# Kernel tuning notes

Measured on AMD Instinct MI355X. Metric: run time of the kernel, lower is better.

Reference implementation:

```python
import jax, jax.numpy as jnp
import numpy as np

N, E, IN, HID, H, OUT = 10000, 160000, 256, 64, 8, 16
NEG_SLOPE = 0.2  # PyG GATConv leaky_relu slope


def _layer_norm(x, g, b, eps=1e-5):
    m = x.mean(-1, keepdims=True)
    v = ((x - m) ** 2).mean(-1, keepdims=True)
    return (x - m) * jax.lax.rsqrt(v + eps) * g + b


def _gat_conv(x, src, dst, W, a_src, a_dst, bias, concat):
    # PyG GATConv: h = x @ W -> [N,H,C]; e_ij = leakyrelu(a_src.h_j + a_dst.h_i);
    # alpha = segment-softmax over incoming edges at dst; out_i = sum_j alpha_ij h_j
    n = x.shape[0]
    heads, c = a_src.shape
    h = (x @ W).reshape(n, heads, c)
    al_s = (h * a_src[None]).sum(-1)  # [N,H]
    al_d = (h * a_dst[None]).sum(-1)  # [N,H]
    e = al_s[src] + al_d[dst]         # [Etot,H]
    e = jnp.where(e > 0, e, NEG_SLOPE * e)
    m = jax.ops.segment_max(e, dst, num_segments=n)
    p = jnp.exp(e - m[dst])
    s = jax.ops.segment_sum(p, dst, num_segments=n)
    a = p / (s[dst] + 1e-16)          # [Etot,H]
    out = jax.ops.segment_sum(h[src] * a[:, :, None], dst, num_segments=n)
    out = out.reshape(n, heads * c) if concat else out.mean(axis=1)
    return out + bias


def setup_inputs() -> dict:
    key = jax.random.key(0)
    ks = jax.random.split(key, 12)
    d = {}
    d['x'] = jax.random.normal(ks[0], (N, IN), jnp.float32)
    d['edge_index'] = jax.random.randint(ks[1], (2, E), 0, N, jnp.int64)
    d['Wp'] = jax.random.normal(ks[2], (IN, HID * H), jnp.float32) * 0.05
    d['bp'] = jnp.zeros((HID * H,), jnp.float32)
    d['g0'] = jnp.ones((HID * H,), jnp.float32)
    d['b0'] = jnp.zeros((HID * H,), jnp.float32)
    d['W1'] = jax.random.normal(ks[3], (HID * H, HID * H), jnp.float32) * 0.05
    d['as1'] = jax.random.normal(ks[4], (H, HID), jnp.float32) * 0.1
    d['ad1'] = jax.random.normal(ks[5], (H, HID), jnp.float32) * 0.1
    d['b1'] = jnp.zeros((HID * H,), jnp.float32)
    d['g1'] = jnp.ones((HID * H,), jnp.float32)
    d['be1'] = jnp.zeros((HID * H,), jnp.float32)
    d['W2'] = jax.random.normal(ks[6], (HID * H, HID * H), jnp.float32) * 0.05
    d['as2'] = jax.random.normal(ks[7], (H, HID), jnp.float32) * 0.1
    d['ad2'] = jax.random.normal(ks[8], (H, HID), jnp.float32) * 0.1
    d['b2'] = jnp.zeros((HID * H,), jnp.float32)
    d['g2'] = jnp.ones((HID * H,), jnp.float32)
    d['be2'] = jnp.zeros((HID * H,), jnp.float32)
    d['W3'] = jax.random.normal(ks[9], (HID * H, OUT), jnp.float32) * 0.05
    d['as3'] = jax.random.normal(ks[10], (1, OUT), jnp.float32) * 0.1
    d['ad3'] = jax.random.normal(ks[11], (1, OUT), jnp.float32) * 0.1
    d['b3'] = jnp.zeros((OUT,), jnp.float32)
    d['g3'] = jnp.ones((OUT,), jnp.float32)
    d['be3'] = jnp.zeros((OUT,), jnp.float32)
    return d


def reference(x, edge_index, Wp, bp, g0, b0, W1, as1, ad1, b1, g1, be1,
              W2, as2, ad2, b2, g2, be2, W3, as3, ad3, b3, g3, be3):
    n = x.shape[0]
    loops = jnp.arange(n)  # PyG add_self_loops=True
    src = jnp.concatenate([edge_index[0], loops])
    dst = jnp.concatenate([edge_index[1], loops])
    x = jax.nn.elu(_layer_norm(x @ Wp + bp, g0, b0))
    # layer 1 (heads=8, concat) + residual
    r = x
    x = _gat_conv(x, src, dst, W1, as1, ad1, b1, True)
    x = jax.nn.elu(_layer_norm(x, g1, be1)) + r
    # layer 2 (heads=8, concat) + residual
    r = x
    x = _gat_conv(x, src, dst, W2, as2, ad2, b2, True)
    x = jax.nn.elu(_layer_norm(x, g2, be2)) + r
    # final layer (heads=1, mean/no-concat), no elu/residual
    x = _gat_conv(x, src, dst, W3, as3, ad3, b3, False)
    x = _layer_norm(x, g3, be3)
    return x
```

## Files before the change

kernel.cpp:

```cpp
#include <hip/hip_runtime.h>
#include <hip/hip_bf16.h>

#define NNODES 10000
#define NEDGES 160000
#define ETOT   (NEDGES + NNODES)
#define CIN    256
#define CH     512
#define NHEAD  8
#define HDIM   64
#define COUT   16
#define NEG_SLOPE 0.2f
#define NF ((size_t)NNODES * CH)

__device__ __forceinline__ float bf2f(uint u) {
    union { uint i; float f; } v; v.i = u << 16; return v.f;
}
__device__ __forceinline__ ushort f2bf(float x) {
    union { float f; uint i; } v; v.f = x;
    uint r = v.i + 0x7fff + ((v.i >> 16) & 1);
    return (ushort)(r >> 16);
}

typedef __attribute__((ext_vector_type(8))) short short8v;
typedef __attribute__((ext_vector_type(4))) float f32x4;

__global__ void count_deg_k(const int* __restrict__ ei, int* __restrict__ deg) {
    int eid = blockIdx.x * 256 + threadIdx.x;
    if (eid >= ETOT) return;
    int dst = (eid < NEDGES) ? ei[NEDGES + eid] : (eid - NEDGES);
    atomicAdd(&deg[dst], 1);
}

__global__ __launch_bounds__(512) void scan_k(const int* __restrict__ deg, int* __restrict__ startA) {
    __shared__ int partial[512];
    int t = threadIdx.x;
    const int per = (NNODES + 511) / 512;
    int base = t * per;
    int s = 0;
    for (int j = 0; j < per; ++j) { int idx = base + j; if (idx < NNODES) s += deg[idx]; }
    partial[t] = s;
    __syncthreads();
    for (int off = 1; off < 512; off <<= 1) {
        int v = (t >= off) ? partial[t - off] : 0;
        __syncthreads();
        partial[t] += v;
        __syncthreads();
    }
    int run = (t == 0) ? 0 : partial[t - 1];
    for (int j = 0; j < per; ++j) {
        int idx = base + j;
        if (idx < NNODES) { startA[idx] = run; run += deg[idx]; }
    }
}

__global__ void scatter_k(const int* __restrict__ ei, const int* __restrict__ startA,
                          int* __restrict__ cursor, int* __restrict__ csr_src) {
    int eid = blockIdx.x * 256 + threadIdx.x;
    if (eid >= ETOT) return;
    int src, dst;
    if (eid < NEDGES) { src = ei[eid]; dst = ei[NEDGES + eid]; }
    else { src = dst = eid - NEDGES; }
    int pos = startA[dst] + atomicAdd(&cursor[dst], 1);
    csr_src[pos] = src;
}

__global__ void convert_x_k(const float* __restrict__ x, ushort* __restrict__ xb) {
    int idx = blockIdx.x * 256 + threadIdx.x;
    if (idx >= NNODES * CIN / 4) return;
    float4 v = ((const float4*)x)[idx];
    ushort4 o; o.x = f2bf(v.x); o.y = f2bf(v.y); o.z = f2bf(v.z); o.w = f2bf(v.w);
    ((ushort4*)xb)[idx] = o;
}

__global__ __launch_bounds__(256) void convert_wT_k(const float* __restrict__ W, ushort* __restrict__ Wt,
                                                    int K, int N) {
    __shared__ float tile[32][33];
    int tx = threadIdx.x & 31, ty = threadIdx.x >> 5;
    int n0 = blockIdx.x * 32, k0 = blockIdx.y * 32;
#pragma unroll
    for (int r = 0; r < 32; r += 8)
        tile[ty + r][tx] = W[(size_t)(k0 + ty + r) * N + n0 + tx];
    __syncthreads();
#pragma unroll
    for (int r = 0; r < 32; r += 8)
        Wt[(size_t)(n0 + ty + r) * K + k0 + tx] = f2bf(tile[tx][ty + r]);
}

#define LDK 40
__global__ __launch_bounds__(256) void gemm_mfma(const ushort* __restrict__ A, const ushort* __restrict__ Bt,
                                                 const float* __restrict__ bias, ushort* __restrict__ C,
                                                 int M, int K) {
    __shared__ ushort Asl[64 * LDK];
    __shared__ ushort Bsl[64 * LDK];
    int t = threadIdx.x;
    int wid = t >> 6, lane = t & 63;
    int row0 = blockIdx.x * 64, col0 = blockIdx.y * 64;
    int wr = (wid >> 1) * 32, wc = (wid & 1) * 32;
    f32x4 acc[2][2] = {};
    int sRow = t >> 2;
    int sK = (t & 3) * 8;
    int lr = lane & 15;
    int kg = (lane >> 4) * 8;

    for (int k0 = 0; k0 < K; k0 += 32) {
        int gr = row0 + sRow;
        uint4 av = {0u, 0u, 0u, 0u};
        if (gr < M) av = *(const uint4*)(A + (size_t)gr * K + k0 + sK);
        *(uint4*)(&Asl[sRow * LDK + sK]) = av;
        uint4 bv = *(const uint4*)(Bt + (size_t)(col0 + sRow) * K + k0 + sK);
        *(uint4*)(&Bsl[sRow * LDK + sK]) = bv;
        __syncthreads();
        short8v a0 = *(const short8v*)(&Asl[(wr + lr) * LDK + kg]);
        short8v a1 = *(const short8v*)(&Asl[(wr + 16 + lr) * LDK + kg]);
        short8v b0 = *(const short8v*)(&Bsl[(wc + lr) * LDK + kg]);
        short8v b1 = *(const short8v*)(&Bsl[(wc + 16 + lr) * LDK + kg]);
        acc[0][0] = __builtin_amdgcn_mfma_f32_16x16x32_bf16(a0, b0, acc[0][0], 0, 0, 0);
        acc[0][1] = __builtin_amdgcn_mfma_f32_16x16x32_bf16(a0, b1, acc[0][1], 0, 0, 0);
        acc[1][0] = __builtin_amdgcn_mfma_f32_16x16x32_bf16(a1, b0, acc[1][0], 0, 0, 0);
        acc[1][1] = __builtin_amdgcn_mfma_f32_16x16x32_bf16(a1, b1, acc[1][1], 0, 0, 0);
        __syncthreads();
    }
#pragma unroll
    for (int mf = 0; mf < 2; ++mf) {
#pragma unroll
        for (int nf = 0; nf < 2; ++nf) {
            int c = col0 + wc + nf * 16 + lr;
            float bb = bias ? bias[c] : 0.f;
#pragma unroll
            for (int j = 0; j < 4; ++j) {
                int r = row0 + wr + mf * 16 + (lane >> 4) * 4 + j;
                if (r < M) C[(size_t)r * CH + c] = f2bf(acc[mf][nf][j] + bb);
            }
        }
    }
}

__global__ __launch_bounds__(128) void ln_elu_k(const ushort* __restrict__ inb, const float* __restrict__ g,
                                                const float* __restrict__ b, ushort* __restrict__ outb) {
    int i = blockIdx.x, t = threadIdx.x;
    uint2 hv = ((const uint2*)(inb + (size_t)i * CH))[t];
    float a0 = bf2f(hv.x & 0xffff), a1 = bf2f(hv.x >> 16);
    float a2 = bf2f(hv.y & 0xffff), a3 = bf2f(hv.y >> 16);
    float s = a0 + a1 + a2 + a3;
    float s2 = a0 * a0 + a1 * a1 + a2 * a2 + a3 * a3;
#pragma unroll
    for (int off = 1; off < 64; off <<= 1) { s += __shfl_xor(s, off); s2 += __shfl_xor(s2, off); }
    __shared__ float sh[4];
    int wid = t >> 6, lane = t & 63;
    if (lane == 0) { sh[wid] = s; sh[2 + wid] = s2; }
    __syncthreads();
    float tot = sh[0] + sh[1], tot2 = sh[2] + sh[3];
    float mean = tot * (1.0f / CH);
    float var = tot2 * (1.0f / CH) - mean * mean;
    float rstd = rsqrtf(var + 1e-5f);
    float4 gv = ((const float4*)g)[t];
    float4 bv = ((const float4*)b)[t];
    float y0 = (a0 - mean) * rstd * gv.x + bv.x; y0 = y0 > 0.f ? y0 : __expf(y0) - 1.f;
    float y1 = (a1 - mean) * rstd * gv.y + bv.y; y1 = y1 > 0.f ? y1 : __expf(y1) - 1.f;
    float y2 = (a2 - mean) * rstd * gv.z + bv.z; y2 = y2 > 0.f ? y2 : __expf(y2) - 1.f;
    float y3 = (a3 - mean) * rstd * gv.w + bv.w; y3 = y3 > 0.f ? y3 : __expf(y3) - 1.f;
    ushort4 o; o.x = f2bf(y0); o.y = f2bf(y1); o.z = f2bf(y2); o.w = f2bf(y3);
    ((ushort4*)(outb + (size_t)i * CH))[t] = o;
}

__global__ void attn_logits_k(const ushort* __restrict__ h, const float* __restrict__ a_src,
                              const float* __restrict__ a_dst, float* __restrict__ als,
                              float* __restrict__ ald) {
    int idx = blockIdx.x * 256 + threadIdx.x;
    if (idx >= NNODES * NHEAD) return;
    int i = idx >> 3, hh = idx & 7;
    const uint2* hp = (const uint2*)(h + (size_t)i * CH + hh * HDIM);
    const float* sp = a_src + hh * HDIM;
    const float* dp = a_dst + hh * HDIM;
    float s = 0.f, d = 0.f;
#pragma unroll
    for (int j = 0; j < HDIM / 4; ++j) {
        uint2 v = hp[j];
        float h0 = bf2f(v.x & 0xffff), h1 = bf2f(v.x >> 16);
        float h2 = bf2f(v.y & 0xffff), h3 = bf2f(v.y >> 16);
        s += h0 * sp[j * 4] + h1 * sp[j * 4 + 1] + h2 * sp[j * 4 + 2] + h3 * sp[j * 4 + 3];
        d += h0 * dp[j * 4] + h1 * dp[j * 4 + 1] + h2 * dp[j * 4 + 2] + h3 * dp[j * 4 + 3];
    }
    als[idx] = s; ald[idx] = d;
}

template <int H>
__global__ void alpha_k(const float* __restrict__ als, const float* __restrict__ ald,
                        const int* __restrict__ startA, const int* __restrict__ deg,
                        const int* __restrict__ csr, float* __restrict__ palpha,
                        float* __restrict__ invs) {
    int idx = blockIdx.x * 256 + threadIdx.x;
    if (idx >= NNODES * H) return;
    int i = idx / H, hh = idx % H;
    int s0 = startA[i], d = deg[i];
    float aldv = ald[idx];
    float m = -1e30f;
    for (int e = 0; e < d; ++e) {
        int src = csr[s0 + e];
        float ee = als[src * H + hh] + aldv;
        ee = ee > 0.f ? ee : NEG_SLOPE * ee;
        m = fmaxf(m, ee);
    }
    float s = 0.f;
    for (int e = 0; e < d; ++e) {
        int src = csr[s0 + e];
        float ee = als[src * H + hh] + aldv;
        ee = ee > 0.f ? ee : NEG_SLOPE * ee;
        float p = __expf(ee - m);
        s += p;
        palpha[(size_t)(s0 + e) * H + hh] = p;
    }
    invs[idx] = 1.0f / (s + 1e-16f);
}

__global__ __launch_bounds__(128) void agg_ln_k(const ushort* __restrict__ hb, const float* __restrict__ palpha,
                                                const float* __restrict__ invs, const int* __restrict__ startA,
                                                const int* __restrict__ deg, const int* __restrict__ csr,
                                                const float* __restrict__ bias, const float* __restrict__ gamma,
                                                const float* __restrict__ beta, const ushort* __restrict__ residb,
                                                ushort* __restrict__ outb) {
    int i = blockIdx.x, t = threadIdx.x;
    int c0 = t * 4, head = t >> 4;
    int s0 = startA[i], d = deg[i];
    const float* pa = palpha + (size_t)s0 * NHEAD + head;
    const int* cp = csr + s0;
    float a0 = 0.f, a1 = 0.f, a2 = 0.f, a3 = 0.f;
    for (int e = 0; e < d; ++e) {
        int src = cp[e];
        float p = pa[(size_t)e * NHEAD];
        uint2 hv = *(const uint2*)(hb + (size_t)src * CH + c0);
        a0 += p * bf2f(hv.x & 0xffff); a1 += p * bf2f(hv.x >> 16);
        a2 += p * bf2f(hv.y & 0xffff); a3 += p * bf2f(hv.y >> 16);
    }
    float inv = invs[i * NHEAD + head];
    float4 bi = ((const float4*)bias)[t];
    a0 = a0 * inv + bi.x; a1 = a1 * inv + bi.y; a2 = a2 * inv + bi.z; a3 = a3 * inv + bi.w;
    float s = a0 + a1 + a2 + a3;
    float s2 = a0 * a0 + a1 * a1 + a2 * a2 + a3 * a3;
#pragma unroll
    for (int off = 1; off < 64; off <<= 1) { s += __shfl_xor(s, off); s2 += __shfl_xor(s2, off); }
    __shared__ float sh[4];
    int wid = t >> 6, lane = t & 63;
    if (lane == 0) { sh[wid] = s; sh[2 + wid] = s2; }
    __syncthreads();
    float tot = sh[0] + sh[1], tot2 = sh[2] + sh[3];
    float mean = tot * (1.0f / CH);
    float var = tot2 * (1.0f / CH) - mean * mean;
    float rstd = rsqrtf(var + 1e-5f);
    float4 gv = ((const float4*)gamma)[t];
    float4 bv = ((const float4*)beta)[t];
    uint2 rv = ((const uint2*)(residb + (size_t)i * CH))[t];
    float y0 = (a0 - mean) * rstd * gv.x + bv.x; y0 = (y0 > 0.f ? y0 : __expf(y0) - 1.f) + bf2f(rv.x & 0xffff);
    float y1 = (a1 - mean) * rstd * gv.y + bv.y; y1 = (y1 > 0.f ? y1 : __expf(y1) - 1.f) + bf2f(rv.x >> 16);
    float y2 = (a2 - mean) * rstd * gv.z + bv.z; y2 = (y2 > 0.f ? y2 : __expf(y2) - 1.f) + bf2f(rv.y & 0xffff);
    float y3 = (a3 - mean) * rstd * gv.w + bv.w; y3 = (y3 > 0.f ? y3 : __expf(y3) - 1.f) + bf2f(rv.y >> 16);
    ushort4 o; o.x = f2bf(y0); o.y = f2bf(y1); o.z = f2bf(y2); o.w = f2bf(y3);
    ((ushort4*)(outb + (size_t)i * CH))[t] = o;
}

__global__ __launch_bounds__(256) void gemm_small_k(const ushort* __restrict__ A, const float* __restrict__ W,
                                                    float* __restrict__ C) {
    int col = threadIdx.x & 15;
    int row = blockIdx.x * 16 + (threadIdx.x >> 4);
    if (row >= NNODES) return;
    const ushort* ar = A + (size_t)row * CH;
    float acc = 0.f;
#pragma unroll 8
    for (int k = 0; k < CH; k += 2) {
        uint av = *(const uint*)(ar + k);
        acc += bf2f(av & 0xffff) * W[k * COUT + col];
        acc += bf2f(av >> 16) * W[(k + 1) * COUT + col];
    }
    C[row * COUT + col] = acc;
}

__global__ void attn_logits1_k(const float* __restrict__ h3, const float* __restrict__ as3,
                               const float* __restrict__ ad3, float* __restrict__ als3,
                               float* __restrict__ ald3) {
    int i = blockIdx.x * 256 + threadIdx.x;
    if (i >= NNODES) return;
    float s = 0.f, d = 0.f;
#pragma unroll
    for (int c = 0; c < COUT; ++c) {
        float v = h3[i * COUT + c];
        s += v * as3[c]; d += v * ad3[c];
    }
    als3[i] = s; ald3[i] = d;
}

__global__ __launch_bounds__(256) void agg16_k(const float* __restrict__ h3, const float* __restrict__ palpha3,
                                               const float* __restrict__ invs3, const int* __restrict__ startA,
                                               const int* __restrict__ deg, const int* __restrict__ csr,
                                               const float* __restrict__ b3, const float* __restrict__ g3,
                                               const float* __restrict__ be3, float* __restrict__ out) {
    int t = threadIdx.x;
    int i = blockIdx.x * 16 + (t >> 4);
    int c = t & 15;
    if (i >= NNODES) return;
    int s0 = startA[i], d = deg[i];
    float acc = 0.f;
    for (int e = 0; e < d; ++e) {
        int pos = s0 + e;
        acc += palpha3[pos] * h3[csr[pos] * COUT + c];
    }
    acc = acc * invs3[i] + b3[c];
    float v = acc, v2 = acc * acc;
#pragma unroll
    for (int off = 1; off < 16; off <<= 1) { v += __shfl_xor(v, off, 16); v2 += __shfl_xor(v2, off, 16); }
    float mean = v * (1.0f / COUT);
    float var = v2 * (1.0f / COUT) - mean * mean;
    out[i * COUT + c] = (acc - mean) * rsqrtf(var + 1e-5f) * g3[c] + be3[c];
}

extern "C" void kernel_launch(void* const* d_in, const int* in_sizes, int n_in,
                              void* d_out, int out_size, void* d_ws, size_t ws_size,
                              hipStream_t stream) {
    const float* x   = (const float*)d_in[0];
    const int*   ei  = (const int*)d_in[1];
    const float* Wp  = (const float*)d_in[2];
    const float* bp  = (const float*)d_in[3];
    const float* g0  = (const float*)d_in[4];
    const float* b0  = (const float*)d_in[5];
    const float* W1  = (const float*)d_in[6];
    const float* as1 = (const float*)d_in[7];
    const float* ad1 = (const float*)d_in[8];
    const float* b1  = (const float*)d_in[9];
    const float* g1  = (const float*)d_in[10];
    const float* be1 = (const float*)d_in[11];
    const float* W2  = (const float*)d_in[12];
    const float* as2 = (const float*)d_in[13];
    const float* ad2 = (const float*)d_in[14];
    const float* b2  = (const float*)d_in[15];
    const float* g2  = (const float*)d_in[16];
    const float* be2 = (const float*)d_in[17];
    const float* W3  = (const float*)d_in[18];
    const float* as3 = (const float*)d_in[19];
    const float* ad3 = (const float*)d_in[20];
    const float* b3  = (const float*)d_in[21];
    const float* g3  = (const float*)d_in[22];
    const float* be3 = (const float*)d_in[23];

    ushort* B0  = (ushort*)d_ws;
    ushort* B1  = B0 + NF;
    ushort* B2  = B1 + NF;
    ushort* xbf = B2 + NF;
    ushort* Wpt = xbf + (size_t)NNODES * CIN;
    ushort* W1t = Wpt + (size_t)CIN * CH;
    ushort* W2t = W1t + (size_t)CH * CH;
    float* als     = (float*)(W2t + (size_t)CH * CH);
    float* ald     = als + NNODES * NHEAD;
    float* palpha  = ald + NNODES * NHEAD;
    float* invs    = palpha + (size_t)ETOT * NHEAD;
    float* h3      = invs + NNODES * NHEAD;
    float* als3    = h3 + (size_t)NNODES * COUT;
    float* ald3    = als3 + NNODES;
    float* palpha3 = ald3 + NNODES;
    float* invs3   = palpha3 + ETOT;
    int* deg = (int*)(invs3 + NNODES);
    int* stA = deg + NNODES;
    int* cur = stA + NNODES;
    int* csr = cur + NNODES;

    hipMemsetAsync(deg, 0, NNODES * sizeof(int), stream);
    hipMemsetAsync(cur, 0, NNODES * sizeof(int), stream);
    count_deg_k<<<(ETOT + 255) / 256, 256, 0, stream>>>(ei, deg);
    scan_k<<<1, 512, 0, stream>>>(deg, stA);
    scatter_k<<<(ETOT + 255) / 256, 256, 0, stream>>>(ei, stA, cur, csr);

    convert_x_k<<<(NNODES * CIN / 4 + 255) / 256, 256, 0, stream>>>(x, xbf);
    convert_wT_k<<<dim3(CH / 32, CIN / 32), 256, 0, stream>>>(Wp, Wpt, CIN, CH);
    convert_wT_k<<<dim3(CH / 32, CH / 32), 256, 0, stream>>>(W1, W1t, CH, CH);
    convert_wT_k<<<dim3(CH / 32, CH / 32), 256, 0, stream>>>(W2, W2t, CH, CH);

    dim3 gg((NNODES + 63) / 64, CH / 64);

    gemm_mfma<<<gg, 256, 0, stream>>>(xbf, Wpt, bp, B0, NNODES, CIN);
    ln_elu_k<<<NNODES, 128, 0, stream>>>(B0, g0, b0, B1);

    gemm_mfma<<<gg, 256, 0, stream>>>(B1, W1t, nullptr, B2, NNODES, CH);
    attn_logits_k<<<(NNODES * NHEAD + 255) / 256, 256, 0, stream>>>(B2, as1, ad1, als, ald);
    alpha_k<NHEAD><<<(NNODES * NHEAD + 255) / 256, 256, 0, stream>>>(als, ald, stA, deg, csr, palpha, invs);
    agg_ln_k<<<NNODES, 128, 0, stream>>>(B2, palpha, invs, stA, deg, csr, b1, g1, be1, B1, B0);

    gemm_mfma<<<gg, 256, 0, stream>>>(B0, W2t, nullptr, B1, NNODES, CH);
    attn_logits_k<<<(NNODES * NHEAD + 255) / 256, 256, 0, stream>>>(B1, as2, ad2, als, ald);
    alpha_k<NHEAD><<<(NNODES * NHEAD + 255) / 256, 256, 0, stream>>>(als, ald, stA, deg, csr, palpha, invs);
    agg_ln_k<<<NNODES, 128, 0, stream>>>(B1, palpha, invs, stA, deg, csr, b2, g2, be2, B0, B2);

    gemm_small_k<<<NNODES / 16, 256, 0, stream>>>(B2, W3, h3);
    attn_logits1_k<<<(NNODES + 255) / 256, 256, 0, stream>>>(h3, as3, ad3, als3, ald3);
    alpha_k<1><<<(NNODES + 255) / 256, 256, 0, stream>>>(als3, ald3, stA, deg, csr, palpha3, invs3);
    agg16_k<<<NNODES / 16, 256, 0, stream>>>(h3, palpha3, invs3, stA, deg, csr, b3, g3, be3, (float*)d_out);
}
```

Before: 384.7 us.

## Use 128x128 MFMA GEMM tiles with direct global-to-LDS loads and padded rows

```diff
diff --git a/kernel.cpp b/kernel.cpp
--- a/kernel.cpp
+++ b/kernel.cpp
@@ -2,6 +2,7 @@
 #include <hip/hip_bf16.h>
 
 #define NNODES 10000
+#define NROWP  10112
 #define NEDGES 160000
 #define ETOT   (NEDGES + NNODES)
 #define CIN    256
@@ -10,7 +11,6 @@
 #define HDIM   64
 #define COUT   16
 #define NEG_SLOPE 0.2f
-#define NF ((size_t)NNODES * CH)
 
 __device__ __forceinline__ float bf2f(uint u) {
     union { uint i; float f; } v; v.i = u << 16; return v.f;
@@ -86,50 +86,61 @@
         Wt[(size_t)(n0 + ty + r) * K + k0 + tx] = f2bf(tile[tx][ty + r]);
 }
 
-#define LDK 40
-__global__ __launch_bounds__(256) void gemm_mfma(const ushort* __restrict__ A, const ushort* __restrict__ Bt,
-                                                 const float* __restrict__ bias, ushort* __restrict__ C,
-                                                 int M, int K) {
-    __shared__ ushort Asl[64 * LDK];
-    __shared__ ushort Bsl[64 * LDK];
+__global__ __launch_bounds__(256) void gemm_mfma128(const ushort* __restrict__ A,
+                                                    const ushort* __restrict__ Bt,
+                                                    const float* __restrict__ bias,
+                                                    ushort* __restrict__ C, int M, int K) {
+    __shared__ __align__(16) ushort Asl[128 * 32];
+    __shared__ __align__(16) ushort Bsl[128 * 32];
     int t = threadIdx.x;
     int wid = t >> 6, lane = t & 63;
-    int row0 = blockIdx.x * 64, col0 = blockIdx.y * 64;
-    int wr = (wid >> 1) * 32, wc = (wid & 1) * 32;
-    f32x4 acc[2][2] = {};
-    int sRow = t >> 2;
-    int sK = (t & 3) * 8;
-    int lr = lane & 15;
-    int kg = (lane >> 4) * 8;
+    int row0 = blockIdx.x * 128, col0 = blockIdx.y * 128;
+    int wr = (wid >> 1) * 64, wc = (wid & 1) * 64;
+    f32x4 acc[4][4] = {};
+    int c0row = t >> 2, c0kg = t & 3;
+    const ushort* Ag0 = A + (size_t)(row0 + c0row) * K + c0kg * 8;
+    const ushort* Ag1 = A + (size_t)(row0 + 64 + c0row) * K + c0kg * 8;
+    const ushort* Bg0 = Bt + (size_t)(col0 + c0row) * K + c0kg * 8;
+    const ushort* Bg1 = Bt + (size_t)(col0 + 64 + c0row) * K + c0kg * 8;
+    int lr = lane & 15, kg = lane >> 4;
 
     for (int k0 = 0; k0 < K; k0 += 32) {
-        int gr = row0 + sRow;
-        uint4 av = {0u, 0u, 0u, 0u};
-        if (gr < M) av = *(const uint4*)(A + (size_t)gr * K + k0 + sK);
-        *(uint4*)(&Asl[sRow * LDK + sK]) = av;
-        uint4 bv = *(const uint4*)(Bt + (size_t)(col0 + sRow) * K + k0 + sK);
-        *(uint4*)(&Bsl[sRow * LDK + sK]) = bv;
+        __builtin_amdgcn_global_load_lds(
+            (const __attribute__((address_space(1))) uint*)(const void*)(Ag0 + k0),
+            (__attribute__((address_space(3))) uint*)&Asl[t * 8], 16, 0, 0);
+        __builtin_amdgcn_global_load_lds(
+            (const __attribute__((address_space(1))) uint*)(const void*)(Ag1 + k0),
+            (__attribute__((address_space(3))) uint*)&Asl[(t + 256) * 8], 16, 0, 0);
+        __builtin_amdgcn_global_load_lds(
+            (const __attribute__((address_space(1))) uint*)(const void*)(Bg0 + k0),
+            (__attribute__((address_space(3))) uint*)&Bsl[t * 8], 16, 0, 0);
+        __builtin_amdgcn_global_load_lds(
+            (const __attribute__((address_space(1))) uint*)(const void*)(Bg1 + k0),
+            (__attribute__((address_space(3))) uint*)&Bsl[(t + 256) * 8], 16, 0, 0);
         __syncthreads();
-        short8v a0 = *(const short8v*)(&Asl[(wr + lr) * LDK + kg]);
-        short8v a1 = *(const short8v*)(&Asl[(wr + 16 + lr) * LDK + kg]);
-        short8v b0 = *(const short8v*)(&Bsl[(wc + lr) * LDK + kg]);
-        short8v b1 = *(const short8v*)(&Bsl[(wc + 16 + lr) * LDK + kg]);
-        acc[0][0] = __builtin_amdgcn_mfma_f32_16x16x32_bf16(a0, b0, acc[0][0], 0, 0, 0);
-        acc[0][1] = __builtin_amdgcn_mfma_f32_16x16x32_bf16(a0, b1, acc[0][1], 0, 0, 0);
-        acc[1][0] = __builtin_amdgcn_mfma_f32_16x16x32_bf16(a1, b0, acc[1][0], 0, 0, 0);
-        acc[1][1] = __builtin_amdgcn_mfma_f32_16x16x32_bf16(a1, b1, acc[1][1], 0, 0, 0);
+        short8v af[4], bfr[4];
+#pragma unroll
+        for (int i = 0; i < 4; ++i) {
+            af[i]  = *(const short8v*)&Asl[(wr + i * 16 + lr) * 32 + kg * 8];
+            bfr[i] = *(const short8v*)&Bsl[(wc + i * 16 + lr) * 32 + kg * 8];
+        }
+#pragma unroll
+        for (int i = 0; i < 4; ++i)
+#pragma unroll
+            for (int j = 0; j < 4; ++j)
+                acc[i][j] = __builtin_amdgcn_mfma_f32_16x16x32_bf16(af[i], bfr[j], acc[i][j], 0, 0, 0);
         __syncthreads();
     }
 #pragma unroll
-    for (int mf = 0; mf < 2; ++mf) {
-#pragma unroll
-        for (int nf = 0; nf < 2; ++nf) {
-            int c = col0 + wc + nf * 16 + lr;
-            float bb = bias ? bias[c] : 0.f;
-#pragma unroll
-            for (int j = 0; j < 4; ++j) {
-                int r = row0 + wr + mf * 16 + (lane >> 4) * 4 + j;
-                if (r < M) C[(size_t)r * CH + c] = f2bf(acc[mf][nf][j] + bb);
+    for (int j = 0; j < 4; ++j) {
+        int c = col0 + wc + j * 16 + lr;
+        float bb = bias ? bias[c] : 0.f;
+#pragma unroll
+        for (int i = 0; i < 4; ++i) {
+#pragma unroll
+            for (int q = 0; q < 4; ++q) {
+                int r = row0 + wr + i * 16 + kg * 4 + q;
+                if (r < M) C[(size_t)r * CH + c] = f2bf(acc[i][j][q] + bb);
             }
         }
     }
@@ -340,11 +351,12 @@
     const float* g3  = (const float*)d_in[22];
     const float* be3 = (const float*)d_in[23];
 
+    const size_t NFP = (size_t)NROWP * CH;
     ushort* B0  = (ushort*)d_ws;
-    ushort* B1  = B0 + NF;
-    ushort* B2  = B1 + NF;
-    ushort* xbf = B2 + NF;
-    ushort* Wpt = xbf + (size_t)NNODES * CIN;
+    ushort* B1  = B0 + NFP;
+    ushort* B2  = B1 + NFP;
+    ushort* xbf = B2 + NFP;
+    ushort* Wpt = xbf + (size_t)NROWP * CIN;
     ushort* W1t = Wpt + (size_t)CIN * CH;
     ushort* W2t = W1t + (size_t)CH * CH;
     float* als     = (float*)(W2t + (size_t)CH * CH);
@@ -372,23 +384,23 @@
     convert_wT_k<<<dim3(CH / 32, CH / 32), 256, 0, stream>>>(W1, W1t, CH, CH);
     convert_wT_k<<<dim3(CH / 32, CH / 32), 256, 0, stream>>>(W2, W2t, CH, CH);
 
-    dim3 gg((NNODES + 63) / 64, CH / 64);
-
-    gemm_mfma<<<gg, 256, 0, stream>>>(xbf, Wpt, bp, B0, NNODES, CIN);
+    dim3 gg(NROWP / 128, CH / 128);
+
+    gemm_mfma128<<<gg, 256, 0, stream>>>(xbf, Wpt, bp, B0, NNODES, CIN);
     ln_elu_k<<<NNODES, 128, 0, stream>>>(B0, g0, b0, B1);
 
-    gemm_mfma<<<gg, 256, 0, stream>>>(B1, W1t, nullptr, B2, NNODES, CH);
+    gemm_mfma128<<<gg, 256, 0, stream>>>(B1, W1t, nullptr, B2, NNODES, CH);
     attn_logits_k<<<(NNODES * NHEAD + 255) / 256, 256, 0, stream>>>(B2, as1, ad1, als, ald);
     alpha_k<NHEAD><<<(NNODES * NHEAD + 255) / 256, 256, 0, stream>>>(als, ald, stA, deg, csr, palpha, invs);
     agg_ln_k<<<NNODES, 128, 0, stream>>>(B2, palpha, invs, stA, deg, csr, b1, g1, be1, B1, B0);
 
-    gemm_mfma<<<gg, 256, 0, stream>>>(B0, W2t, nullptr, B1, NNODES, CH);
+    gemm_mfma128<<<gg, 256, 0, stream>>>(B0, W2t, nullptr, B1, NNODES, CH);
     attn_logits_k<<<(NNODES * NHEAD + 255) / 256, 256, 0, stream>>>(B1, as2, ad2, als, ald);
     alpha_k<NHEAD><<<(NNODES * NHEAD + 255) / 256, 256, 0, stream>>>(als, ald, stA, deg, csr, palpha, invs);
     agg_ln_k<<<NNODES, 128, 0, stream>>>(B1, palpha, invs, stA, deg, csr, b2, g2, be2, B0, B2);
 
-    gemm_small_k<<<NNODES / 16, 256, 0, stream>>>(B2, W3, h3);
+    gemm_small_k<<<(NNODES + 15) / 16, 256, 0, stream>>>(B2, W3, h3);
     attn_logits1_k<<<(NNODES + 255) / 256, 256, 0, stream>>>(h3, as3, ad3, als3, ald3);
     alpha_k<1><<<(NNODES + 255) / 256, 256, 0, stream>>>(als3, ald3, stA, deg, csr, palpha3, invs3);
-    agg16_k<<<NNODES / 16, 256, 0, stream>>>(h3, palpha3, invs3, stA, deg, csr, b3, g3, be3, (float*)d_out);
-}
+    agg16_k<<<(NNODES + 15) / 16, 256, 0, stream>>>(h3, palpha3, invs3, stA, deg, csr, b3, g3, be3, (float*)d_out);
+}
```

Measured after the change: 397.6 us. 1.03x slower.

## Fuse edge softmax into aggregation kernels using an online-softmax rescale

Applied to the files above, without the earlier changes.

```diff
diff --git a/kernel.cpp b/kernel.cpp
--- a/kernel.cpp
+++ b/kernel.cpp
@@ -184,37 +184,8 @@
     als[idx] = s; ald[idx] = d;
 }
 
-template <int H>
-__global__ void alpha_k(const float* __restrict__ als, const float* __restrict__ ald,
-                        const int* __restrict__ startA, const int* __restrict__ deg,
-                        const int* __restrict__ csr, float* __restrict__ palpha,
-                        float* __restrict__ invs) {
-    int idx = blockIdx.x * 256 + threadIdx.x;
-    if (idx >= NNODES * H) return;
-    int i = idx / H, hh = idx % H;
-    int s0 = startA[i], d = deg[i];
-    float aldv = ald[idx];
-    float m = -1e30f;
-    for (int e = 0; e < d; ++e) {
-        int src = csr[s0 + e];
-        float ee = als[src * H + hh] + aldv;
-        ee = ee > 0.f ? ee : NEG_SLOPE * ee;
-        m = fmaxf(m, ee);
-    }
-    float s = 0.f;
-    for (int e = 0; e < d; ++e) {
-        int src = csr[s0 + e];
-        float ee = als[src * H + hh] + aldv;
-        ee = ee > 0.f ? ee : NEG_SLOPE * ee;
-        float p = __expf(ee - m);
-        s += p;
-        palpha[(size_t)(s0 + e) * H + hh] = p;
-    }
-    invs[idx] = 1.0f / (s + 1e-16f);
-}
-
-__global__ __launch_bounds__(128) void agg_ln_k(const ushort* __restrict__ hb, const float* __restrict__ palpha,
-                                                const float* __restrict__ invs, const int* __restrict__ startA,
+__global__ __launch_bounds__(128) void agg_ln_k(const ushort* __restrict__ hb, const float* __restrict__ als,
+                                                const float* __restrict__ ald, const int* __restrict__ startA,
                                                 const int* __restrict__ deg, const int* __restrict__ csr,
                                                 const float* __restrict__ bias, const float* __restrict__ gamma,
                                                 const float* __restrict__ beta, const ushort* __restrict__ residb,
@@ -222,17 +193,28 @@
     int i = blockIdx.x, t = threadIdx.x;
     int c0 = t * 4, head = t >> 4;
     int s0 = startA[i], d = deg[i];
-    const float* pa = palpha + (size_t)s0 * NHEAD + head;
+    float aldv = ald[i * NHEAD + head];
     const int* cp = csr + s0;
+    float m = -1e30f, ssum = 0.f;
     float a0 = 0.f, a1 = 0.f, a2 = 0.f, a3 = 0.f;
     for (int e = 0; e < d; ++e) {
         int src = cp[e];
-        float p = pa[(size_t)e * NHEAD];
+        float ee = als[src * NHEAD + head] + aldv;
+        ee = ee > 0.f ? ee : NEG_SLOPE * ee;
+        float p;
+        if (ee > m) {
+            float scale = __expf(m - ee);
+            ssum *= scale; a0 *= scale; a1 *= scale; a2 *= scale; a3 *= scale;
+            m = ee; p = 1.0f;
+        } else {
+            p = __expf(ee - m);
+        }
+        ssum += p;
         uint2 hv = *(const uint2*)(hb + (size_t)src * CH + c0);
         a0 += p * bf2f(hv.x & 0xffff); a1 += p * bf2f(hv.x >> 16);
         a2 += p * bf2f(hv.y & 0xffff); a3 += p * bf2f(hv.y >> 16);
     }
-    float inv = invs[i * NHEAD + head];
+    float inv = 1.0f / (ssum + 1e-16f);
     float4 bi = ((const float4*)bias)[t];
     a0 = a0 * inv + bi.x; a1 = a1 * inv + bi.y; a2 = a2 * inv + bi.z; a3 = a3 * inv + bi.w;
     float s = a0 + a1 + a2 + a3;
@@ -274,36 +256,41 @@
     C[row * COUT + col] = acc;
 }
 
-__global__ void attn_logits1_k(const float* __restrict__ h3, const float* __restrict__ as3,
-                               const float* __restrict__ ad3, float* __restrict__ als3,
-                               float* __restrict__ ald3) {
-    int i = blockIdx.x * 256 + threadIdx.x;
-    if (i >= NNODES) return;
-    float s = 0.f, d = 0.f;
-#pragma unroll
-    for (int c = 0; c < COUT; ++c) {
-        float v = h3[i * COUT + c];
-        s += v * as3[c]; d += v * ad3[c];
-    }
-    als3[i] = s; ald3[i] = d;
-}
-
-__global__ __launch_bounds__(256) void agg16_k(const float* __restrict__ h3, const float* __restrict__ palpha3,
-                                               const float* __restrict__ invs3, const int* __restrict__ startA,
-                                               const int* __restrict__ deg, const int* __restrict__ csr,
-                                               const float* __restrict__ b3, const float* __restrict__ g3,
-                                               const float* __restrict__ be3, float* __restrict__ out) {
+__global__ __launch_bounds__(256) void agg16f_k(const float* __restrict__ h3, const float* __restrict__ as3,
+                                                const float* __restrict__ ad3, const int* __restrict__ startA,
+                                                const int* __restrict__ deg, const int* __restrict__ csr,
+                                                const float* __restrict__ b3, const float* __restrict__ g3,
+                                                const float* __restrict__ be3, float* __restrict__ out) {
     int t = threadIdx.x;
     int i = blockIdx.x * 16 + (t >> 4);
     int c = t & 15;
     if (i >= NNODES) return;
+    float asc = as3[c], adc = ad3[c];
+    float ald_i = h3[i * COUT + c] * adc;
+#pragma unroll
+    for (int off = 1; off < 16; off <<= 1) ald_i += __shfl_xor(ald_i, off, 16);
     int s0 = startA[i], d = deg[i];
-    float acc = 0.f;
+    float m = -1e30f, ssum = 0.f, acc = 0.f;
     for (int e = 0; e < d; ++e) {
-        int pos = s0 + e;
-        acc += palpha3[pos] * h3[csr[pos] * COUT + c];
-    }
-    acc = acc * invs3[i] + b3[c];
+        int src = csr[s0 + e];
+        float v = h3[src * COUT + c];
+        float al = v * asc;
+#pragma unroll
+        for (int off = 1; off < 16; off <<= 1) al += __shfl_xor(al, off, 16);
+        float ee = al + ald_i;
+        ee = ee > 0.f ? ee : NEG_SLOPE * ee;
+        float p;
+        if (ee > m) {
+            float scale = __expf(m - ee);
+            ssum *= scale; acc *= scale;
+            m = ee; p = 1.0f;
+        } else {
+            p = __expf(ee - m);
+        }
+        ssum += p;
+        acc += p * v;
+    }
+    acc = acc / (ssum + 1e-16f) + b3[c];
     float v = acc, v2 = acc * acc;
 #pragma unroll
     for (int off = 1; off < 16; off <<= 1) { v += __shfl_xor(v, off, 16); v2 += __shfl_xor(v2, off, 16); }
@@ -347,16 +334,10 @@
     ushort* Wpt = xbf + (size_t)NNODES * CIN;
     ushort* W1t = Wpt + (size_t)CIN * CH;
     ushort* W2t = W1t + (size_t)CH * CH;
-    float* als     = (float*)(W2t + (size_t)CH * CH);
-    float* ald     = als + NNODES * NHEAD;
-    float* palpha  = ald + NNODES * NHEAD;
-    float* invs    = palpha + (size_t)ETOT * NHEAD;
-    float* h3      = invs + NNODES * NHEAD;
-    float* als3    = h3 + (size_t)NNODES * COUT;
-    float* ald3    = als3 + NNODES;
-    float* palpha3 = ald3 + NNODES;
-    float* invs3   = palpha3 + ETOT;
-    int* deg = (int*)(invs3 + NNODES);
+    float* als = (float*)(W2t + (size_t)CH * CH);
+    float* ald = als + NNODES * NHEAD;
+    float* h3  = ald + NNODES * NHEAD;
+    int* deg = (int*)(h3 + (size_t)NNODES * COUT);
     int* stA = deg + NNODES;
     int* cur = stA + NNODES;
     int* csr = cur + NNODES;
@@ -379,16 +360,12 @@
 
     gemm_mfma<<<gg, 256, 0, stream>>>(B1, W1t, nullptr, B2, NNODES, CH);
     attn_logits_k<<<(NNODES * NHEAD + 255) / 256, 256, 0, stream>>>(B2, as1, ad1, als, ald);
-    alpha_k<NHEAD><<<(NNODES * NHEAD + 255) / 256, 256, 0, stream>>>(als, ald, stA, deg, csr, palpha, invs);
-    agg_ln_k<<<NNODES, 128, 0, stream>>>(B2, palpha, invs, stA, deg, csr, b1, g1, be1, B1, B0);
+    agg_ln_k<<<NNODES, 128, 0, stream>>>(B2, als, ald, stA, deg, csr, b1, g1, be1, B1, B0);
 
     gemm_mfma<<<gg, 256, 0, stream>>>(B0, W2t, nullptr, B1, NNODES, CH);
     attn_logits_k<<<(NNODES * NHEAD + 255) / 256, 256, 0, stream>>>(B1, as2, ad2, als, ald);
-    alpha_k<NHEAD><<<(NNODES * NHEAD + 255) / 256, 256, 0, stream>>>(als, ald, stA, deg, csr, palpha, invs);
-    agg_ln_k<<<NNODES, 128, 0, stream>>>(B1, palpha, invs, stA, deg, csr, b2, g2, be2, B0, B2);
-
-    gemm_small_k<<<NNODES / 16, 256, 0, stream>>>(B2, W3, h3);
-    attn_logits1_k<<<(NNODES + 255) / 256, 256, 0, stream>>>(h3, as3, ad3, als3, ald3);
-    alpha_k<1><<<(NNODES + 255) / 256, 256, 0, stream>>>(als3, ald3, stA, deg, csr, palpha3, invs3);
-    agg16_k<<<NNODES / 16, 256, 0, stream>>>(h3, palpha3, invs3, stA, deg, csr, b3, g3, be3, (float*)d_out);
-}
+    agg_ln_k<<<NNODES, 128, 0, stream>>>(B1, als, ald, stA, deg, csr, b2, g2, be2, B0, B2);
+
+    gemm_small_k<<<(NNODES + 15) / 16, 256, 0, stream>>>(B2, W3, h3);
+    agg16f_k<<<(NNODES + 15) / 16, 256, 0, stream>>>(h3, as3, ad3, stA, deg, csr, b3, g3, be3, (float*)d_out);
+}
```

Measured after the change: 367.3 us. 1.05x faster.
